# Kernel optimization log

Hardware: AMD Instinct MI355X
Metric: run time of the kernel (lower is better)

The kernel has to match this reference:

```python
import jax, jax.numpy as jnp
import numpy as np
import math

# batch, in-channels, attention_maps, heads, features (== input height), frames
B, C, M, H, F_, W = 2, 8, 8, 8, 256, 512
HD = F_ // H  # head dim = 32


def conv2d(x, w, pad):
    return jax.lax.conv_general_dilated(x, w, (1, 1), pad,
                                        dimension_numbers=('NCHW', 'OIHW', 'NCHW'))


def rotary(x):
    # lucidrains-style interleaved rotary over last dim; x: [..., seq, d]
    d, seq = x.shape[-1], x.shape[-2]
    inv_freq = 1.0 / (10000.0 ** (jnp.arange(0, d, 2, dtype=jnp.float32) / d))
    freqs = jnp.arange(seq, dtype=jnp.float32)[:, None] * inv_freq[None, :]  # [seq, d/2]
    freqs = jnp.repeat(freqs, 2, axis=-1)  # [seq, d], each freq repeated for the (x1,x2) pair
    cos, sin = jnp.cos(freqs), jnp.sin(freqs)
    x1, x2 = x[..., 0::2], x[..., 1::2]
    xr = jnp.stack((-x2, x1), axis=-1).reshape(x.shape)  # rotate_half
    return x * cos + xr * sin


def setup_inputs() -> dict:
    key = jax.random.key(0)
    ks = jax.random.split(key, 12)
    s = 0.02
    return {
        'x': jax.random.normal(ks[0], (B, C, F_, W), jnp.float32),
        'prev_qk': jax.random.normal(ks[1], (B, M, H, W, W), jnp.float32) * 0.1,
        'q_c1': jax.random.normal(ks[2], (M, C, 3, 3), jnp.float32) * s,
        'q_lin': jax.random.normal(ks[3], (M, F_, F_), jnp.float32) * s,
        'q_c2': jax.random.normal(ks[4], (M, M, 1, 3), jnp.float32) * s,
        'k_c1': jax.random.normal(ks[5], (M, C, 3, 3), jnp.float32) * s,
        'k_lin': jax.random.normal(ks[6], (M, F_, F_), jnp.float32) * s,
        'k_c2': jax.random.normal(ks[7], (M, M, 1, 3), jnp.float32) * s,
        'v_c1': jax.random.normal(ks[8], (M, C, 3, 3), jnp.float32) * s,
        'v_lin': jax.random.normal(ks[9], (M, F_, F_), jnp.float32) * s,
        'v_c2': jax.random.normal(ks[10], (M, M, 1, 3), jnp.float32) * s,
        'o_w': jax.random.normal(ks[11], (M, F_, F_), jnp.float32) * s,
    }


def _proj(x, wc1, wl, wc2):
    h = conv2d(x, wc1, [(1, 1), (1, 1)])        # [B,M,F,W] 3x3 conv, no bias
    h = jnp.einsum('bcfw,cgf->bcgw', h, wl)      # MultichannelLinear: per-map linear on feature dim
    h = conv2d(h, wc2, [(0, 0), (1, 1)])         # (1,3) conv along frames
    return h


def _heads(t):
    # [B,M,F,W] -> transpose(2,3) -> [B,M,W,F] -> [B,M,W,H,HD] -> [B,M,H,W,HD]
    return t.transpose(0, 1, 3, 2).reshape(B, M, W, H, HD).transpose(0, 1, 3, 2, 4)


def reference(x, prev_qk, q_c1, q_lin, q_c2, k_c1, k_lin, k_c2, v_c1, v_lin, v_c2, o_w):
    q = rotary(_heads(_proj(x, q_c1, q_lin, q_c2)))
    k = rotary(_heads(_proj(x, k_c1, k_lin, k_c2)))
    v = _heads(_proj(x, v_c1, v_lin, v_c2))
    # scaled by sqrt(h) where h == input height == features (non-standard)
    qk = jnp.einsum('bmhqd,bmhkd->bmhqk', q, k) / math.sqrt(F_) + prev_qk
    a = jnp.einsum('bmhqk,bmhkd->bmhqd', jax.nn.softmax(qk, axis=-1), v)
    a = a.transpose(0, 1, 3, 2, 4).reshape(B, M, W, F_).transpose(0, 1, 3, 2)  # [B,M,F,W]
    out = jnp.einsum('bcfw,cgf->bcgw', a, o_w)  # o_proj MultichannelLinear
    return (out, qk)
```

## Files before the change

### kernel.cpp

```cpp
#include <hip/hip_runtime.h>

#define B 2
#define C 8
#define M 8
#define H 8
#define F 256
#define W 512
#define HD 32
#define MFF (M * F * F)

typedef __attribute__((ext_vector_type(8))) __bf16 bf16x8;
typedef __attribute__((ext_vector_type(4))) float f32x4;

__device__ __forceinline__ unsigned short f2bf(float f) {
    unsigned int u = __float_as_uint(f);
    return (unsigned short)((u + 0x7fffu + ((u >> 16) & 1u)) >> 16);
}

__device__ __forceinline__ unsigned int packsplit(float v) {
    unsigned short h = f2bf(v);
    float hf = __uint_as_float((unsigned int)h << 16);
    unsigned short lo = f2bf(v - hf);
    return (unsigned int)h | ((unsigned int)lo << 16);
}

__global__ __launch_bounds__(256) void wsplit_kernel(const float* __restrict__ w0,
                                                     const float* __restrict__ w1,
                                                     const float* __restrict__ w2,
                                                     const float* __restrict__ w3,
                                                     unsigned short* __restrict__ hi) {
    int idx = blockIdx.x * 256 + threadIdx.x;
    int set = idx >> 17;
    int off = (idx & 131071) * 4;
    const float* src = (set == 0) ? w0 : (set == 1) ? w1 : (set == 2) ? w2 : w3;
    float4 v = *(const float4*)&src[off];
    unsigned short* hp = hi + (size_t)set * MFF + off;
    unsigned short* lp = hp + 4 * MFF;
    ushort4 hv, lv;
    float x;
    x = v.x; hv.x = f2bf(x); lv.x = f2bf(x - __uint_as_float((unsigned)hv.x << 16));
    x = v.y; hv.y = f2bf(x); lv.y = f2bf(x - __uint_as_float((unsigned)hv.y << 16));
    x = v.z; hv.z = f2bf(x); lv.z = f2bf(x - __uint_as_float((unsigned)hv.z << 16));
    x = v.w; hv.w = f2bf(x); lv.w = f2bf(x - __uint_as_float((unsigned)hv.w << 16));
    *(ushort4*)hp = hv;
    *(ushort4*)lp = lv;
}

__global__ __launch_bounds__(256) void conv1_kernel(const float* __restrict__ x,
                                                    const float* __restrict__ w0,
                                                    const float* __restrict__ w1,
                                                    const float* __restrict__ w2,
                                                    unsigned int* __restrict__ out) {
    int t = threadIdx.x;
    int zb = blockIdx.z;
    int b = zb >> 3, m = zb & 7;
    int wi = blockIdx.x * 64 + (t & 63);
    int f0t = blockIdx.y * 32 + (t >> 6) * 8;
    const float* xb = x + (size_t)b * C * F * W;
    const float* wq = w0 + m * 72;
    const float* wk = w1 + m * 72;
    const float* wv = w2 + m * 72;
    int wm = (wi > 0) ? wi - 1 : 0;
    int wp = (wi < W - 1) ? wi + 1 : W - 1;
    bool e0 = (wi > 0), e1 = (wi < W - 1);
    float acc[3][8] = {};
    for (int i = 0; i < 8; ++i) {
        const float* xi = xb + (size_t)i * F * W;
        float v0[10], v1[10], v2[10];
        #pragma unroll
        for (int rr = 0; rr < 10; ++rr) {
            int ff = f0t + rr - 1;
            if (ff >= 0 && ff < F) {
                const float* xr = xi + (size_t)ff * W;
                float a = xr[wm], bb = xr[wi], c = xr[wp];
                v0[rr] = e0 ? a : 0.f;
                v1[rr] = bb;
                v2[rr] = e1 ? c : 0.f;
            } else {
                v0[rr] = 0.f; v1[rr] = 0.f; v2[rr] = 0.f;
            }
        }
        #pragma unroll
        for (int p = 0; p < 3; ++p) {
            const float* wt = ((p == 0) ? wq : (p == 1) ? wk : wv) + i * 9;
            #pragma unroll
            for (int df = 0; df < 3; ++df) {
                float s0 = wt[df * 3 + 0];
                float s1 = wt[df * 3 + 1];
                float s2 = wt[df * 3 + 2];
                #pragma unroll
                for (int ff = 0; ff < 8; ++ff)
                    acc[p][ff] += v0[ff + df] * s0 + v1[ff + df] * s1 + v2[ff + df] * s2;
            }
        }
    }
    #pragma unroll
    for (int p = 0; p < 3; ++p) {
        size_t zo = (size_t)(p * 16 + zb) * F;
        #pragma unroll
        for (int ff = 0; ff < 8; ++ff)
            out[(zo + f0t + ff) * W + wi] = packsplit(acc[p][ff]);
    }
}

__global__ __launch_bounds__(256) void lin_kernel(const unsigned int* __restrict__ in32,
                                                  const unsigned short* __restrict__ whA,
                                                  const unsigned short* __restrict__ whB,
                                                  const unsigned short* __restrict__ whC,
                                                  float* __restrict__ out) {
    __shared__ unsigned int BsH[64][20];
    __shared__ unsigned int BsL[64][20];
    int t = threadIdx.x;
    int z = blockIdx.z;
    int proj = z >> 4, m = z & 7;
    const unsigned short* wh = ((proj == 0) ? whA : (proj == 1) ? whB : whC) + (size_t)m * F * F;
    const unsigned short* wl = wh + 4 * MFF;
    const unsigned int* ib = in32 + (size_t)z * F * W;
    float* ob = out + (size_t)z * F * W;
    int g0 = blockIdx.y * 64, wb0 = blockIdx.x * 64;
    int wv = t >> 6, l = t & 63, lr = l & 15, lg = l >> 4;
    int wgr = wv >> 1, wgc = wv & 1;
    int sp = t & 15;
    int sg = t >> 4;

    uint4 ra, rb;
    ra = *(const uint4*)&ib[(size_t)(2 * sp) * W + wb0 + sg * 4];
    rb = *(const uint4*)&ib[(size_t)(2 * sp + 1) * W + wb0 + sg * 4];

    f32x4 acc[2][2];
    acc[0][0] = (f32x4)0.f; acc[0][1] = (f32x4)0.f;
    acc[1][0] = (f32x4)0.f; acc[1][1] = (f32x4)0.f;

    for (int s = 0; s < 8; ++s) {
        int f0 = s * 32;
        if (s) __syncthreads();
        unsigned int aw[4] = {ra.x, ra.y, ra.z, ra.w};
        unsigned int bw[4] = {rb.x, rb.y, rb.z, rb.w};
        #pragma unroll
        for (int j = 0; j < 4; ++j) {
            BsH[sg * 4 + j][sp] = (aw[j] & 0xFFFFu) | (bw[j] << 16);
            BsL[sg * 4 + j][sp] = (aw[j] >> 16) | (bw[j] & 0xFFFF0000u);
        }
        __syncthreads();
        if (s < 7) {
            ra = *(const uint4*)&ib[(size_t)(f0 + 32 + 2 * sp) * W + wb0 + sg * 4];
            rb = *(const uint4*)&ib[(size_t)(f0 + 32 + 2 * sp + 1) * W + wb0 + sg * 4];
        }
        bf16x8 ah[2], al[2], bh[2], bl[2];
        #pragma unroll
        for (int ti = 0; ti < 2; ++ti) {
            size_t ar = (size_t)(g0 + wgr * 32 + ti * 16 + lr) * F + f0 + lg * 8;
            ah[ti] = *(const bf16x8*)&wh[ar];
            al[ti] = *(const bf16x8*)&wl[ar];
        }
        #pragma unroll
        for (int tj = 0; tj < 2; ++tj) {
            int wc = wgc * 32 + tj * 16 + lr;
            bh[tj] = *(const bf16x8*)((const unsigned short*)&BsH[wc][0] + lg * 8);
            bl[tj] = *(const bf16x8*)((const unsigned short*)&BsL[wc][0] + lg * 8);
        }
        #pragma unroll
        for (int ti = 0; ti < 2; ++ti)
            #pragma unroll
            for (int tj = 0; tj < 2; ++tj) {
                acc[ti][tj] = __builtin_amdgcn_mfma_f32_16x16x32_bf16(ah[ti], bh[tj], acc[ti][tj], 0, 0, 0);
                acc[ti][tj] = __builtin_amdgcn_mfma_f32_16x16x32_bf16(ah[ti], bl[tj], acc[ti][tj], 0, 0, 0);
                acc[ti][tj] = __builtin_amdgcn_mfma_f32_16x16x32_bf16(al[ti], bh[tj], acc[ti][tj], 0, 0, 0);
            }
    }
    #pragma unroll
    for (int ti = 0; ti < 2; ++ti)
        #pragma unroll
        for (int tj = 0; tj < 2; ++tj)
            #pragma unroll
            for (int r = 0; r < 4; ++r) {
                int g = g0 + wgr * 32 + ti * 16 + lg * 4 + r;
                int w = wb0 + wgc * 32 + tj * 16 + lr;
                ob[(size_t)g * W + w] = acc[ti][tj][r];
            }
}

__global__ __launch_bounds__(256) void conv2_heads_kernel(const float* __restrict__ in,
                                                          const float* __restrict__ w0c,
                                                          const float* __restrict__ w1c,
                                                          const float* __restrict__ w2c,
                                                          unsigned short* __restrict__ outp) {
    __shared__ float wl[192];
    __shared__ float Ot[64][65];
    int t = threadIdx.x;
    int z = blockIdx.z;
    int proj = z >> 4, bz = z & 15;
    int b = bz >> 3, o = bz & 7;
    const float* wt = (proj == 0) ? w0c : (proj == 1) ? w1c : w2c;
    int do_rot = (proj < 2);
    if (t < 192) wl[t] = wt[t];
    __syncthreads();
    int f0 = blockIdx.y * 64, w0 = blockIdx.x * 64;
    const float* ib = in + ((size_t)proj * 16 + (size_t)b * M) * F * W;
    int wgi = t & 15, fr = t >> 4;
    int wq = w0 + wgi * 4;
    bool eL = (wq > 0);
    bool eR = (wq + 4 < W);
    #pragma unroll
    for (int fi = 0; fi < 4; ++fi) {
        int f = f0 + fr * 4 + fi;
        float a0 = 0.f, a1 = 0.f, a2 = 0.f, a3 = 0.f;
        #pragma unroll
        for (int i = 0; i < 8; ++i) {
            const float* r = ib + ((size_t)i * F + f) * W + wq;
            float4 v = *(const float4*)r;
            float vlft = eL ? r[-1] : 0.f;
            float vrgt = eR ? r[4] : 0.f;
            const float* wr = &wl[(o * 8 + i) * 3];
            float c0 = wr[0], c1 = wr[1], c2 = wr[2];
            a0 += vlft * c0 + v.x * c1 + v.y * c2;
            a1 += v.x  * c0 + v.y * c1 + v.z * c2;
            a2 += v.y  * c0 + v.z * c1 + v.w * c2;
            a3 += v.z  * c0 + v.w * c1 + vrgt * c2;
        }
        Ot[fr * 4 + fi][wgi * 4 + 0] = a0;
        Ot[fr * 4 + fi][wgi * 4 + 1] = a1;
        Ot[fr * 4 + fi][wgi * 4 + 2] = a2;
        Ot[fr * 4 + fi][wgi * 4 + 3] = a3;
    }
    __syncthreads();
    size_t zbase = (size_t)z * H * W * HD;
    if (do_rot) {
        for (int k = 0; k < 16; ++k) {
            int idx = k * 256 + t;
            int ddh = idx & 63;
            int wi = idx >> 6;
            int f = f0 + ddh;
            int h = f >> 5, d = f & 31;
            float e  = Ot[ddh & ~1][wi];
            float od = Ot[ddh | 1][wi];
            int jp = d >> 1;
            float invf = exp2f(-(float)jp * 0.83048202372184058f);
            float th = (float)(w0 + wi) * invf;
            float cs = __cosf(th), sn = __sinf(th);
            float val = (d & 1) ? (od * cs + e * sn) : (e * cs - od * sn);
            outp[zbase + ((size_t)h * W + (w0 + wi)) * HD + d] = f2bf(val);
        }
    } else {
        for (int k = 0; k < 16; ++k) {
            int idx = k * 256 + t;
            int wi = idx & 63;
            int ddh = idx >> 6;
            int f = f0 + ddh;
            int h = f >> 5, d = f & 31;
            outp[zbase + ((size_t)(h * HD + d)) * W + (w0 + wi)] = f2bf(Ot[ddh][wi]);
        }
    }
}

__global__ __launch_bounds__(256) void attn_kernel(const unsigned short* __restrict__ qb,
                                                   const unsigned short* __restrict__ kb,
                                                   const unsigned short* __restrict__ vtb,
                                                   const float* __restrict__ prev,
                                                   float* __restrict__ qk,
                                                   unsigned int* __restrict__ abuf) {
    __shared__ __align__(16) unsigned short VsT[32 * 520];
    __shared__ __align__(16) unsigned short PT[4][16 * 72];
    int t = threadIdx.x;
    int l = t & 63, wv = t >> 6;
    int lr = l & 15, lg = l >> 4;
    int Lid = blockIdx.x;
    int bmh = (Lid & 7) * 16 + ((Lid >> 3) & 15);
    int wbase = (Lid >> 7) * 128;
    const unsigned short* Q  = qb  + (size_t)bmh * W * HD;
    const unsigned short* K  = kb  + (size_t)bmh * W * HD;
    const unsigned short* VT = vtb + (size_t)bmh * HD * W;
    const float* P0 = prev + (size_t)bmh * W * W;
    float* QK = qk + (size_t)bmh * W * W;
    int bm = bmh >> 3, h = bmh & 7;
    unsigned int* A = abuf + ((size_t)bm * F + h * HD) * W;

    #pragma unroll
    for (int it = 0; it < 8; ++it) {
        int e16 = it * 256 + t;
        int hd = e16 >> 6, w8 = (e16 & 63) * 8;
        *(uint4*)&VsT[hd * 520 + w8] = *(const uint4*)&VT[(size_t)hd * W + w8];
    }
    __syncthreads();

    for (int half = 0; half < 2; ++half) {
        int w0 = wbase + half * 64;
        int qrow = w0 + wv * 16;
        bf16x8 qf = *(const bf16x8*)&Q[(size_t)(qrow + lr) * HD + lg * 8];

        float l_i[4] = {0.f, 0.f, 0.f, 0.f};
        f32x4 accA[2];
        accA[0] = (f32x4)0.f;
        accA[1] = (f32x4)0.f;

        bf16x8 kfA[4], kfB[4];
        f32x4 pvA[4], pvB[4];

        auto issue = [&](bf16x8 (&kf)[4], f32x4 (&pv)[4], int c) {
            int j0 = c * 64;
            #pragma unroll
            for (int ct = 0; ct < 4; ++ct)
                kf[ct] = *(const bf16x8*)&K[(size_t)(j0 + ct * 16 + lr) * HD + lg * 8];
            #pragma unroll
            for (int ct = 0; ct < 4; ++ct) {
                const float* pr = &P0[(size_t)(qrow + lg * 4) * W + j0 + ct * 16 + lr];
                #pragma unroll
                for (int r = 0; r < 4; ++r) pv[ct][r] = pr[(size_t)r * W];
            }
        };

        auto step = [&](bf16x8 (&kf)[4], f32x4 (&pv)[4], int c) {
            int j0 = c * 64;
            f32x4 sc[4];
            #pragma unroll
            for (int ct = 0; ct < 4; ++ct)
                sc[ct] = __builtin_amdgcn_mfma_f32_16x16x32_bf16(qf, kf[ct], pv[ct] * 16.f, 0, 0, 0);
            float p[4][4];
            #pragma unroll
            for (int ct = 0; ct < 4; ++ct) {
                #pragma unroll
                for (int r = 0; r < 4; ++r) {
                    float s = sc[ct][r] * 0.0625f;
                    QK[(size_t)(qrow + lg * 4 + r) * W + j0 + ct * 16 + lr] = s;
                    p[ct][r] = __expf(s);
                }
            }
            #pragma unroll
            for (int r = 0; r < 4; ++r)
                l_i[r] += (p[0][r] + p[1][r]) + (p[2][r] + p[3][r]);
            unsigned short* PTw = &PT[wv][0];
            #pragma unroll
            for (int ct = 0; ct < 4; ++ct)
                #pragma unroll
                for (int r = 0; r < 4; ++r)
                    PTw[(lg * 4 + r) * 72 + ct * 16 + lr] = f2bf(p[ct][r]);
            asm volatile("s_waitcnt lgkmcnt(0)" ::: "memory");
            __builtin_amdgcn_sched_barrier(0);
            bf16x8 pf[2];
            pf[0] = *(const bf16x8*)&PTw[lr * 72 + lg * 8];
            pf[1] = *(const bf16x8*)&PTw[lr * 72 + 32 + lg * 8];
            #pragma unroll
            for (int ks = 0; ks < 2; ++ks)
                #pragma unroll
                for (int ct2 = 0; ct2 < 2; ++ct2) {
                    bf16x8 vf = *(const bf16x8*)&VsT[(ct2 * 16 + lr) * 520 + j0 + ks * 32 + lg * 8];
                    accA[ct2] = __builtin_amdgcn_mfma_f32_16x16x32_bf16(pf[ks], vf, accA[ct2], 0, 0, 0);
                }
        };

        issue(kfA, pvA, 0);
        #pragma unroll
        for (int cc = 0; cc < 4; ++cc) {
            issue(kfB, pvB, 2 * cc + 1);
            step(kfA, pvA, 2 * cc);
            if (cc < 3) issue(kfA, pvA, 2 * cc + 2);
            step(kfB, pvB, 2 * cc + 1);
        }

        float inv[4];
        #pragma unroll
        for (int r = 0; r < 4; ++r) {
            float s = l_i[r];
            #pragma unroll
            for (int off = 1; off < 16; off <<= 1) s += __shfl_xor(s, off);
            inv[r] = 1.f / s;
        }
        float* Otf = (float*)&PT[wv][0];
        asm volatile("s_waitcnt lgkmcnt(0)" ::: "memory");
        #pragma unroll
        for (int ct2 = 0; ct2 < 2; ++ct2)
            #pragma unroll
            for (int r = 0; r < 4; ++r)
                Otf[(lg * 4 + r) * 33 + ct2 * 16 + lr] = accA[ct2][r] * inv[r];
        asm volatile("s_waitcnt lgkmcnt(0)" ::: "memory");
        __builtin_amdgcn_sched_barrier(0);
        #pragma unroll
        for (int k = 0; k < 8; ++k) {
            int flat = k * 64 + l;
            int woff = flat & 15, d = flat >> 4;
            A[(size_t)d * W + w0 + wv * 16 + woff] = packsplit(Otf[woff * 33 + d]);
        }
        asm volatile("s_waitcnt lgkmcnt(0)" ::: "memory");
        __builtin_amdgcn_sched_barrier(0);
    }
}

extern "C" void kernel_launch(void* const* d_in, const int* in_sizes, int n_in,
                              void* d_out, int out_size, void* d_ws, size_t ws_size,
                              hipStream_t stream) {
    const float* x    = (const float*)d_in[0];
    const float* prev = (const float*)d_in[1];
    const float* qc1  = (const float*)d_in[2];
    const float* qlin = (const float*)d_in[3];
    const float* qc2  = (const float*)d_in[4];
    const float* kc1  = (const float*)d_in[5];
    const float* klin = (const float*)d_in[6];
    const float* kc2  = (const float*)d_in[7];
    const float* vc1  = (const float*)d_in[8];
    const float* vlin = (const float*)d_in[9];
    const float* vc2  = (const float*)d_in[10];
    const float* ow   = (const float*)d_in[11];
    float* out0  = (float*)d_out;
    float* qkout = out0 + (size_t)B * M * F * W;
    float* ws = (float*)d_ws;
    size_t n = (size_t)B * M * F * W;
    float* r1 = ws;
    float* r2 = ws + 3 * n;
    unsigned int* r1u = (unsigned int*)r1;
    unsigned int* r2u = (unsigned int*)r2;
    unsigned short* qkv16 = (unsigned short*)r1;
    unsigned short* whi = (unsigned short*)(ws + 6 * n);

    dim3 blk(256);
    dim3 gsplit(2048), gconv1(8, 8, 16), glin3(8, 4, 48), gconv2(8, 4, 48);
    dim3 gattn(512), glin1(8, 4, 16);

    wsplit_kernel<<<gsplit, blk, 0, stream>>>(qlin, klin, vlin, ow, whi);
    conv1_kernel<<<gconv1, blk, 0, stream>>>(x, qc1, kc1, vc1, r1u);
    lin_kernel<<<glin3, blk, 0, stream>>>(r1u, whi, whi + MFF, whi + 2 * MFF, r2);
    conv2_heads_kernel<<<gconv2, blk, 0, stream>>>(r2, qc2, kc2, vc2, qkv16);
    attn_kernel<<<gattn, blk, 0, stream>>>(qkv16, qkv16 + n, qkv16 + 2 * n, prev, qkout, r2u);
    lin_kernel<<<glin1, blk, 0, stream>>>(r2u, whi + 3 * MFF, whi + 3 * MFF, whi + 3 * MFF, out0);
}
```

Measured before the change: 402.8 us.

## Enlarge lin_kernel tile to 128 rows and use nontemporal loads/stores in attention

The lin_kernel output tile per block grows from 64x64 to 128x64. Each wave now owns 32 rows across all 64 columns, so every staged B tile in LDS is reused by twice as many output rows and the grid halves along the row axis. Separately, the attention kernel's prev_qk reads and qk output writes become nontemporal, so these streaming accesses pollute the cache less. The cost is more accumulator registers per thread and fewer blocks for the larger tile, which may reduce occupancy and latency hiding.

Result: faster. 380.0 us (-5.7%).

```diff
diff --git a/kernel.cpp b/kernel.cpp
--- a/kernel.cpp
+++ b/kernel.cpp
@@ -117,9 +117,9 @@
     const unsigned short* wl = wh + 4 * MFF;
     const unsigned int* ib = in32 + (size_t)z * F * W;
     float* ob = out + (size_t)z * F * W;
-    int g0 = blockIdx.y * 64, wb0 = blockIdx.x * 64;
+    int g0 = blockIdx.y * 128, wb0 = blockIdx.x * 64;
     int wv = t >> 6, l = t & 63, lr = l & 15, lg = l >> 4;
-    int wgr = wv >> 1, wgc = wv & 1;
+    int gw = g0 + wv * 32;
     int sp = t & 15;
     int sg = t >> 4;
 
@@ -127,9 +127,11 @@
     ra = *(const uint4*)&ib[(size_t)(2 * sp) * W + wb0 + sg * 4];
     rb = *(const uint4*)&ib[(size_t)(2 * sp + 1) * W + wb0 + sg * 4];
 
-    f32x4 acc[2][2];
-    acc[0][0] = (f32x4)0.f; acc[0][1] = (f32x4)0.f;
-    acc[1][0] = (f32x4)0.f; acc[1][1] = (f32x4)0.f;
+    f32x4 acc[2][4];
+    #pragma unroll
+    for (int ti = 0; ti < 2; ++ti)
+        #pragma unroll
+        for (int tj = 0; tj < 4; ++tj) acc[ti][tj] = (f32x4)0.f;
 
     for (int s = 0; s < 8; ++s) {
         int f0 = s * 32;
@@ -146,36 +148,34 @@
             ra = *(const uint4*)&ib[(size_t)(f0 + 32 + 2 * sp) * W + wb0 + sg * 4];
             rb = *(const uint4*)&ib[(size_t)(f0 + 32 + 2 * sp + 1) * W + wb0 + sg * 4];
         }
-        bf16x8 ah[2], al[2], bh[2], bl[2];
+        bf16x8 ah[2], al[2];
         #pragma unroll
         for (int ti = 0; ti < 2; ++ti) {
-            size_t ar = (size_t)(g0 + wgr * 32 + ti * 16 + lr) * F + f0 + lg * 8;
+            size_t ar = (size_t)(gw + ti * 16 + lr) * F + f0 + lg * 8;
             ah[ti] = *(const bf16x8*)&wh[ar];
             al[ti] = *(const bf16x8*)&wl[ar];
         }
         #pragma unroll
-        for (int tj = 0; tj < 2; ++tj) {
-            int wc = wgc * 32 + tj * 16 + lr;
-            bh[tj] = *(const bf16x8*)((const unsigned short*)&BsH[wc][0] + lg * 8);
-            bl[tj] = *(const bf16x8*)((const unsigned short*)&BsL[wc][0] + lg * 8);
-        }
-        #pragma unroll
-        for (int ti = 0; ti < 2; ++ti)
-            #pragma unroll
-            for (int tj = 0; tj < 2; ++tj) {
-                acc[ti][tj] = __builtin_amdgcn_mfma_f32_16x16x32_bf16(ah[ti], bh[tj], acc[ti][tj], 0, 0, 0);
-                acc[ti][tj] = __builtin_amdgcn_mfma_f32_16x16x32_bf16(ah[ti], bl[tj], acc[ti][tj], 0, 0, 0);
-                acc[ti][tj] = __builtin_amdgcn_mfma_f32_16x16x32_bf16(al[ti], bh[tj], acc[ti][tj], 0, 0, 0);
-            }
+        for (int tj = 0; tj < 4; ++tj) {
+            int wc = tj * 16 + lr;
+            bf16x8 bh = *(const bf16x8*)((const unsigned short*)&BsH[wc][0] + lg * 8);
+            bf16x8 bl = *(const bf16x8*)((const unsigned short*)&BsL[wc][0] + lg * 8);
+            #pragma unroll
+            for (int ti = 0; ti < 2; ++ti) {
+                acc[ti][tj] = __builtin_amdgcn_mfma_f32_16x16x32_bf16(ah[ti], bh, acc[ti][tj], 0, 0, 0);
+                acc[ti][tj] = __builtin_amdgcn_mfma_f32_16x16x32_bf16(ah[ti], bl, acc[ti][tj], 0, 0, 0);
+                acc[ti][tj] = __builtin_amdgcn_mfma_f32_16x16x32_bf16(al[ti], bh, acc[ti][tj], 0, 0, 0);
+            }
+        }
     }
     #pragma unroll
     for (int ti = 0; ti < 2; ++ti)
         #pragma unroll
-        for (int tj = 0; tj < 2; ++tj)
+        for (int tj = 0; tj < 4; ++tj)
             #pragma unroll
             for (int r = 0; r < 4; ++r) {
-                int g = g0 + wgr * 32 + ti * 16 + lg * 4 + r;
-                int w = wb0 + wgc * 32 + tj * 16 + lr;
+                int g = gw + ti * 16 + lg * 4 + r;
+                int w = wb0 + tj * 16 + lr;
                 ob[(size_t)g * W + w] = acc[ti][tj][r];
             }
 }
@@ -305,7 +305,7 @@
             for (int ct = 0; ct < 4; ++ct) {
                 const float* pr = &P0[(size_t)(qrow + lg * 4) * W + j0 + ct * 16 + lr];
                 #pragma unroll
-                for (int r = 0; r < 4; ++r) pv[ct][r] = pr[(size_t)r * W];
+                for (int r = 0; r < 4; ++r) pv[ct][r] = __builtin_nontemporal_load(&pr[(size_t)r * W]);
             }
         };
 
@@ -321,7 +321,8 @@
                 #pragma unroll
                 for (int r = 0; r < 4; ++r) {
                     float s = sc[ct][r] * 0.0625f;
-                    QK[(size_t)(qrow + lg * 4 + r) * W + j0 + ct * 16 + lr] = s;
+                    __builtin_nontemporal_store(s,
+                        &QK[(size_t)(qrow + lg * 4 + r) * W + j0 + ct * 16 + lr]);
                     p[ct][r] = __expf(s);
                 }
             }
@@ -412,8 +413,8 @@
     unsigned short* whi = (unsigned short*)(ws + 6 * n);
 
     dim3 blk(256);
-    dim3 gsplit(2048), gconv1(8, 8, 16), glin3(8, 4, 48), gconv2(8, 4, 48);
-    dim3 gattn(512), glin1(8, 4, 16);
+    dim3 gsplit(2048), gconv1(8, 8, 16), glin3(8, 2, 48), gconv2(8, 4, 48);
+    dim3 gattn(512), glin1(8, 2, 16);
 
     wsplit_kernel<<<gsplit, blk, 0, stream>>>(qlin, klin, vlin, ow, whi);
     conv1_kernel<<<gconv1, blk, 0, stream>>>(x, qc1, kc1, vc1, r1u);
```
